# Kernel optimization log

Hardware: AMD Instinct MI355X
Metric: run time of the kernel (lower is better)

Reference implementation:

```python
import jax, jax.numpy as jnp
import numpy as np


def setup_inputs() -> dict:
    key = jax.random.key(0)
    k1, k2, k3 = jax.random.split(key, 3)
    n, seq_len, hidden = 100000, 4, 128
    n_edges = 1600000
    semantics = jax.random.normal(k1, (n, seq_len, hidden), dtype=jnp.float32)
    attention_masks = jnp.ones((n, seq_len, hidden), dtype=jnp.float32)
    W = jax.random.normal(k2, (hidden, hidden), dtype=jnp.float32) * (1.0 / np.sqrt(hidden))
    edge_index = jax.random.randint(k3, (n_edges, 2), 0, n, dtype=jnp.int64)
    return {"semantics": semantics, "attention_masks": attention_masks, "W": W, "edge_index": edge_index}


def reference(semantics, attention_masks, W, edge_index):
    # semantics: (n, seq_len, hidden); only token 0 is used.
    # edge_index: (E, 2) = adj.nonzero(); col 0 = source (gather), col 1 = target (scatter).
    n = semantics.shape[0]
    h = semantics[:, 0] @ W                         # (n, hidden)
    src = h[edge_index[:, 0]]                       # (E, hidden) gather
    tgt = edge_index[:, 1]
    sums = jax.ops.segment_sum(src, tgt, num_segments=n)            # (n, hidden)
    cnt = jax.ops.segment_sum(jnp.ones((edge_index.shape[0],), dtype=h.dtype), tgt, num_segments=n)
    h_mean = sums / jnp.maximum(cnt, 1.0)[:, None]  # scatter_mean; untouched rows stay 0
    return jax.nn.gelu(h_mean, approximate=False)
```

## Files before the change

kernel.cpp:

```cpp
#include <hip/hip_runtime.h>
#include <math.h>


#define SLOT 64

__device__ __forceinline__ float gelu_exact(float x) {
    return 0.5f * x * (1.0f + erff(x * 0.70710678118654752f));
}
__device__ __forceinline__ void fma4(float m, const float4 w, float4& a) {
    a.x = fmaf(m, w.x, a.x); a.y = fmaf(m, w.y, a.y);
    a.z = fmaf(m, w.z, a.z); a.w = fmaf(m, w.w, a.w);
}

__global__ __launch_bounds__(256) void fill_and_matmul(
        const int* __restrict__ edges, int* __restrict__ cnt,
        int* __restrict__ csr, int n_edges,
        const float* __restrict__ sem, const float* __restrict__ W,
        float* __restrict__ h, int n, int mm_blocks) {
    __shared__ float ml[64 * 128];

    int bid = blockIdx.x;
    if (bid % 7 != 0) {
        int fb = bid - bid / 7 - 1;
        int e  = fb * 256 + (int)threadIdx.x;
        if (e < n_edges) {
            int2 p = ((const int2*)edges)[e];
            int pos = atomicAdd(&cnt[p.y], 1);
            if (pos < SLOT) csr[(size_t)p.y * SLOT + pos] = p.x;
        }
        return;
    }

    int mb = bid / 7;
    const int cg = threadIdx.x & 31;
    const int rb = threadIdx.x >> 5;
    const int rowsPerIter = 64 * mm_blocks;

    for (int row0 = mb * 64; row0 < n; row0 += rowsPerIter) {
        __syncthreads();
        #pragma unroll
        for (int p = 0; p < 8; p++) {
            int fid = threadIdx.x + 256 * p;
            int rr = fid >> 5, k4 = fid & 31;
            int row = row0 + rr;
            if (row < n)
                ((float4*)ml)[fid] = ((const float4*)(sem + (size_t)row * 512))[k4];
        }
        __syncthreads();

        float4 acc[8];
        #pragma unroll
        for (int i = 0; i < 8; i++) acc[i] = make_float4(0.f, 0.f, 0.f, 0.f);

        const float* mbase = ml + rb * 8 * 128;

        for (int kc = 0; kc < 16; kc++) {
            float4 wreg[8];
            #pragma unroll
            for (int u = 0; u < 8; u++)
                wreg[u] = ((const float4*)(W + (size_t)(kc * 8 + u) * 128))[cg];
            #pragma unroll
            for (int rr = 0; rr < 8; rr++) {
                const float4* mrow = (const float4*)(mbase + rr * 128);
                float4 mlo = mrow[kc * 2], mhi = mrow[kc * 2 + 1];
                fma4(mlo.x, wreg[0], acc[rr]);
                fma4(mlo.y, wreg[1], acc[rr]);
                fma4(mlo.z, wreg[2], acc[rr]);
                fma4(mlo.w, wreg[3], acc[rr]);
                fma4(mhi.x, wreg[4], acc[rr]);
                fma4(mhi.y, wreg[5], acc[rr]);
                fma4(mhi.z, wreg[6], acc[rr]);
                fma4(mhi.w, wreg[7], acc[rr]);
            }
        }

        #pragma unroll
        for (int rr = 0; rr < 8; rr++) {
            int row = row0 + rb * 8 + rr;
            if (row < n)
                ((float4*)(h + (size_t)row * 128))[cg] = acc[rr];
        }
    }
}

__global__ __launch_bounds__(256) void gather_gelu(
        const float* __restrict__ h, const int* __restrict__ cnt,
        const int* __restrict__ csr, float* __restrict__ out, int n) {
    int gid  = blockIdx.x * blockDim.x + threadIdx.x;
    int node = gid >> 6;
    int lane = gid & 63;
    if (node >= n) return;

    int deg = cnt[node];
    int m   = min(deg, SLOT);
    int sv  = (lane < m) ? csr[(size_t)node * SLOT + lane] : 0;

    const int half = lane >> 5;
    const int q    = lane & 31;

    float4 acc = make_float4(0.f, 0.f, 0.f, 0.f);

    int j = 0;
    for (; j + 16 <= m; j += 16) {
        int s[8];
        #pragma unroll
        for (int u = 0; u < 8; u++) s[u] = __shfl(sv, j + 2 * u + half);
        float4 v[8];
        #pragma unroll
        for (int u = 0; u < 8; u++)
            v[u] = ((const float4*)(h + (size_t)s[u] * 128))[q];
        #pragma unroll
        for (int u = 0; u < 8; u++) {
            acc.x += v[u].x; acc.y += v[u].y; acc.z += v[u].z; acc.w += v[u].w;
        }
    }
    for (; j + 2 <= m; j += 2) {
        int s = __shfl(sv, j + half);
        float4 v = ((const float4*)(h + (size_t)s * 128))[q];
        acc.x += v.x; acc.y += v.y; acc.z += v.z; acc.w += v.w;
    }
    if (j < m) {
        int s = __shfl(sv, j);
        if (half == 0) {
            float4 v = ((const float4*)(h + (size_t)s * 128))[q];
            acc.x += v.x; acc.y += v.y; acc.z += v.z; acc.w += v.w;
        }
    }

    float4 oth;
    oth.x = __shfl(acc.x, (lane + 32) & 63);
    oth.y = __shfl(acc.y, (lane + 32) & 63);
    oth.z = __shfl(acc.z, (lane + 32) & 63);
    oth.w = __shfl(acc.w, (lane + 32) & 63);

    if (half == 0) {
        float inv = 1.0f / fmaxf((float)deg, 1.0f);
        float4 t = make_float4(gelu_exact((acc.x + oth.x) * inv),
                               gelu_exact((acc.y + oth.y) * inv),
                               gelu_exact((acc.z + oth.z) * inv),
                               gelu_exact((acc.w + oth.w) * inv));
        ((float4*)(out + (size_t)node * 128))[q] = t;
    }
}

extern "C" void kernel_launch(void* const* d_in, const int* in_sizes, int n_in,
                              void* d_out, int out_size, void* d_ws, size_t ws_size,
                              hipStream_t stream) {
    const float* sem   = (const float*)d_in[0];
    const float* W     = (const float*)d_in[2];
    const int*   edges = (const int*)d_in[3];

    const int n       = in_sizes[0] / (4 * 128);
    const int n_edges = in_sizes[3] / 2;

    auto align16 = [](size_t x) { return (x + 15) & ~(size_t)15; };
    char* p = (char*)d_ws;
    int*   cnt = (int*)p;    p += align16((size_t)n * 4);
    int*   csr = (int*)p;    p += align16((size_t)n * SLOT * 4);
    float* h   = (float*)p;

    hipMemsetAsync(cnt, 0, (size_t)n * 4, stream);

    const int T  = 256;
    const int FB = (n_edges + T - 1) / T;
    const int total = (FB * 7 + 5) / 6;
    const int MB    = total - FB;

    fill_and_matmul<<<total, T, 0, stream>>>(edges, cnt, csr, n_edges,
                                             sem, W, h, n, MB);

    const int gblocks = (int)(((long long)n * 64 + T - 1) / T);
    gather_gelu<<<gblocks, T, 0, stream>>>(h, cnt, csr, (float*)d_out, n);
}
```

Before: 553.9 us.

## Split edge list in halves to overlap second CSR fill with first gather

Splits the edges into two halves, each with its own per-node count and 32-slot CSR. The first half is filled alongside the matmul (matmul blocks now come first). The second half is filled inside the same launch that gathers the first half, and a final kernel gathers the second half and applies mean and GELU. The gather loop also becomes branch-free by masking with an FMA in place of the remainder tails. This adds a third launch and an extra write and read of the partial sums through the output buffer, and caps each half at 32 neighbours per node instead of 64 overall.

```diff
diff --git a/kernel.cpp b/kernel.cpp
--- a/kernel.cpp
+++ b/kernel.cpp
@@ -2,7 +2,7 @@
 #include <math.h>
 
 
-#define SLOT 64
+#define SLOT_H 32
 
 __device__ __forceinline__ float gelu_exact(float x) {
     return 0.5f * x * (1.0f + erff(x * 0.70710678118654752f));
@@ -12,31 +12,29 @@
     a.z = fmaf(m, w.z, a.z); a.w = fmaf(m, w.w, a.w);
 }
 
-__global__ __launch_bounds__(256) void fill_and_matmul(
-        const int* __restrict__ edges, int* __restrict__ cnt,
-        int* __restrict__ csr, int n_edges,
+__global__ __launch_bounds__(256) void fill_a_matmul(
+        const int* __restrict__ edges, int* __restrict__ cnt_a,
+        int* __restrict__ csr_a, int e1,
         const float* __restrict__ sem, const float* __restrict__ W,
-        float* __restrict__ h, int n, int mm_blocks) {
+        float* __restrict__ h, int n, int mmb) {
     __shared__ float ml[64 * 128];
 
     int bid = blockIdx.x;
-    if (bid % 7 != 0) {
-        int fb = bid - bid / 7 - 1;
-        int e  = fb * 256 + (int)threadIdx.x;
-        if (e < n_edges) {
+    if (bid >= mmb) {
+        int e = (bid - mmb) * 256 + (int)threadIdx.x;
+        if (e < e1) {
             int2 p = ((const int2*)edges)[e];
-            int pos = atomicAdd(&cnt[p.y], 1);
-            if (pos < SLOT) csr[(size_t)p.y * SLOT + pos] = p.x;
+            int pos = atomicAdd(&cnt_a[p.y], 1);
+            if (pos < SLOT_H) csr_a[(size_t)p.y * SLOT_H + pos] = p.x;
         }
         return;
     }
 
-    int mb = bid / 7;
     const int cg = threadIdx.x & 31;
     const int rb = threadIdx.x >> 5;
-    const int rowsPerIter = 64 * mm_blocks;
-
-    for (int row0 = mb * 64; row0 < n; row0 += rowsPerIter) {
+    const int rowsPerIter = 64 * mmb;
+
+    for (int row0 = bid * 64; row0 < n; row0 += rowsPerIter) {
         __syncthreads();
         #pragma unroll
         for (int p = 0; p < 8; p++) {
@@ -83,63 +81,93 @@
     }
 }
 
-__global__ __launch_bounds__(256) void gather_gelu(
-        const float* __restrict__ h, const int* __restrict__ cnt,
-        const int* __restrict__ csr, float* __restrict__ out, int n) {
-    int gid  = blockIdx.x * blockDim.x + threadIdx.x;
-    int node = gid >> 6;
-    int lane = gid & 63;
-    if (node >= n) return;
-
-    int deg = cnt[node];
-    int m   = min(deg, SLOT);
-    int sv  = (lane < m) ? csr[(size_t)node * SLOT + lane] : 0;
-
-    const int half = lane >> 5;
-    const int q    = lane & 31;
+__device__ __forceinline__ float4 gather_half(
+        const float* __restrict__ h, const int* __restrict__ csr,
+        int node, int m, int lane, int half, int q) {
+    int sv = (lane < m) ? csr[(size_t)node * SLOT_H + lane] : 0;
 
     float4 acc = make_float4(0.f, 0.f, 0.f, 0.f);
-
-    int j = 0;
-    for (; j + 16 <= m; j += 16) {
-        int s[8];
-        #pragma unroll
-        for (int u = 0; u < 8; u++) s[u] = __shfl(sv, j + 2 * u + half);
+    for (int j = 0; j < m; j += 16) {
+        int   ss[8];
+        float mk[8];
+        #pragma unroll
+        for (int u = 0; u < 8; u++) {
+            int idx = j + 2 * u + half;
+            int s   = __shfl(sv, idx & 31);
+            bool on = idx < m;
+            ss[u] = on ? s : 0;
+            mk[u] = on ? 1.f : 0.f;
+        }
         float4 v[8];
         #pragma unroll
         for (int u = 0; u < 8; u++)
-            v[u] = ((const float4*)(h + (size_t)s[u] * 128))[q];
+            v[u] = ((const float4*)(h + (size_t)ss[u] * 128))[q];
         #pragma unroll
         for (int u = 0; u < 8; u++) {
-            acc.x += v[u].x; acc.y += v[u].y; acc.z += v[u].z; acc.w += v[u].w;
-        }
-    }
-    for (; j + 2 <= m; j += 2) {
-        int s = __shfl(sv, j + half);
-        float4 v = ((const float4*)(h + (size_t)s * 128))[q];
-        acc.x += v.x; acc.y += v.y; acc.z += v.z; acc.w += v.w;
-    }
-    if (j < m) {
-        int s = __shfl(sv, j);
-        if (half == 0) {
-            float4 v = ((const float4*)(h + (size_t)s * 128))[q];
-            acc.x += v.x; acc.y += v.y; acc.z += v.z; acc.w += v.w;
-        }
-    }
-
+            acc.x = fmaf(v[u].x, mk[u], acc.x);
+            acc.y = fmaf(v[u].y, mk[u], acc.y);
+            acc.z = fmaf(v[u].z, mk[u], acc.z);
+            acc.w = fmaf(v[u].w, mk[u], acc.w);
+        }
+    }
     float4 oth;
     oth.x = __shfl(acc.x, (lane + 32) & 63);
     oth.y = __shfl(acc.y, (lane + 32) & 63);
     oth.z = __shfl(acc.z, (lane + 32) & 63);
     oth.w = __shfl(acc.w, (lane + 32) & 63);
-
-    if (half == 0) {
-        float inv = 1.0f / fmaxf((float)deg, 1.0f);
-        float4 t = make_float4(gelu_exact((acc.x + oth.x) * inv),
-                               gelu_exact((acc.y + oth.y) * inv),
-                               gelu_exact((acc.z + oth.z) * inv),
-                               gelu_exact((acc.w + oth.w) * inv));
-        ((float4*)(out + (size_t)node * 128))[q] = t;
+    return make_float4(acc.x + oth.x, acc.y + oth.y,
+                       acc.z + oth.z, acc.w + oth.w);
+}
+
+__global__ __launch_bounds__(256) void fill_b_gather_a(
+        const int* __restrict__ edges, int* __restrict__ cnt_b,
+        int* __restrict__ csr_b, int e1, int e2,
+        const float* __restrict__ h, const int* __restrict__ cnt_a,
+        const int* __restrict__ csr_a, float* __restrict__ io,
+        int n, int fb2) {
+    int bid = blockIdx.x;
+    if (bid < fb2) {
+        int e = bid * 256 + (int)threadIdx.x;
+        if (e < e2) {
+            int2 p = ((const int2*)edges)[(size_t)e1 + e];
+            int pos = atomicAdd(&cnt_b[p.y], 1);
+            if (pos < SLOT_H) csr_b[(size_t)p.y * SLOT_H + pos] = p.x;
+        }
+        return;
+    }
+
+    int gid  = (bid - fb2) * 256 + (int)threadIdx.x;
+    int node = gid >> 6;
+    int lane = gid & 63;
+    if (node >= n) return;
+
+    int m = min(cnt_a[node], SLOT_H);
+    float4 s = gather_half(h, csr_a, node, m, lane, lane >> 5, lane & 31);
+    if (lane < 32)
+        ((float4*)(io + (size_t)node * 128))[lane] = s;
+}
+
+__global__ __launch_bounds__(256) void gather_b_final(
+        const float* __restrict__ h, const int* __restrict__ cnt_a,
+        const int* __restrict__ cnt_b, const int* __restrict__ csr_b,
+        float* __restrict__ io, int n) {
+    int gid  = blockIdx.x * blockDim.x + threadIdx.x;
+    int node = gid >> 6;
+    int lane = gid & 63;
+    if (node >= n) return;
+
+    int ca = cnt_a[node], cb = cnt_b[node];
+    int m = min(cb, SLOT_H);
+    float4 s = gather_half(h, csr_b, node, m, lane, lane >> 5, lane & 31);
+
+    if (lane < 32) {
+        float4 part = ((const float4*)(io + (size_t)node * 128))[lane];
+        float inv = 1.0f / fmaxf((float)(ca + cb), 1.0f);
+        float4 t = make_float4(gelu_exact((s.x + part.x) * inv),
+                               gelu_exact((s.y + part.y) * inv),
+                               gelu_exact((s.z + part.z) * inv),
+                               gelu_exact((s.w + part.w) * inv));
+        ((float4*)(io + (size_t)node * 128))[lane] = t;
     }
 }
 
@@ -152,23 +180,30 @@
 
     const int n       = in_sizes[0] / (4 * 128);
     const int n_edges = in_sizes[3] / 2;
+    const int e1      = n_edges / 2;
+    const int e2      = n_edges - e1;
 
     auto align16 = [](size_t x) { return (x + 15) & ~(size_t)15; };
     char* p = (char*)d_ws;
-    int*   cnt = (int*)p;    p += align16((size_t)n * 4);
-    int*   csr = (int*)p;    p += align16((size_t)n * SLOT * 4);
-    float* h   = (float*)p;
-
-    hipMemsetAsync(cnt, 0, (size_t)n * 4, stream);
-
-    const int T  = 256;
-    const int FB = (n_edges + T - 1) / T;
-    const int total = (FB * 7 + 5) / 6;
-    const int MB    = total - FB;
-
-    fill_and_matmul<<<total, T, 0, stream>>>(edges, cnt, csr, n_edges,
-                                             sem, W, h, n, MB);
-
-    const int gblocks = (int)(((long long)n * 64 + T - 1) / T);
-    gather_gelu<<<gblocks, T, 0, stream>>>(h, cnt, csr, (float*)d_out, n);
-}
+    int*   cnt_a = (int*)p;  p += align16((size_t)n * 4);
+    int*   cnt_b = (int*)p;  p += align16((size_t)n * 4);
+    int*   csr_a = (int*)p;  p += align16((size_t)n * SLOT_H * 4);
+    int*   csr_b = (int*)p;  p += align16((size_t)n * SLOT_H * 4);
+    float* h     = (float*)p;
+
+    hipMemsetAsync(cnt_a, 0, 2 * align16((size_t)n * 4), stream);
+
+    const int T   = 256;
+    const int MMB = 1024;
+    const int FB1 = (e1 + T - 1) / T;
+    const int FB2 = (e2 + T - 1) / T;
+    const int GB  = (int)(((long long)n * 64 + T - 1) / T);
+
+    fill_a_matmul  <<<MMB + FB1, T, 0, stream>>>(edges, cnt_a, csr_a, e1,
+                                                 sem, W, h, n, MMB);
+    fill_b_gather_a<<<FB2 + GB,  T, 0, stream>>>(edges, cnt_b, csr_b, e1, e2,
+                                                 h, cnt_a, csr_a,
+                                                 (float*)d_out, n, FB2);
+    gather_b_final <<<GB,        T, 0, stream>>>(h, cnt_a, cnt_b, csr_b,
+                                                 (float*)d_out, n);
+}
```

Measured after the change: 587.7 us. +6.1%, slower.
